# Optimization experiments

Measured on AMD Instinct MI355X. Metric: run time of the kernel, lower is better.

Reference implementation:

```python
import jax, jax.numpy as jnp
import numpy as np

DIM = 512
HEADS = 8
DK = DIM // HEADS
MAX_LEN = 22118
EPS = 1e-5


def _layernorm(h, g, b):
    m = jnp.mean(h, axis=-1, keepdims=True)
    v = jnp.mean((h - m) ** 2, axis=-1, keepdims=True)
    return (h - m) / jnp.sqrt(v + EPS) * g + b


def setup_inputs() -> dict:
    key = jax.random.key(0)
    ks = jax.random.split(key, 16)
    B, S = 4, 2048
    xavier = lambda k, shp: jax.random.normal(k, shp, jnp.float32) * np.sqrt(2.0 / (shp[0] + shp[1]))
    return {
        "x": jax.random.normal(ks[0], (B, S, DIM), jnp.float32),
        "vis_data": jax.random.normal(ks[1], (B, S, DIM), jnp.float32),
        "coord1": jax.random.randint(ks[2], (B, S), 0, MAX_LEN, jnp.int32),
        "coord2": jax.random.randint(ks[3], (B, S), 0, MAX_LEN, jnp.int32),
        "emb1": jax.random.normal(ks[4], (MAX_LEN, DIM // 2), jnp.float32) * 0.02,
        "emb2": jax.random.normal(ks[5], (MAX_LEN, DIM // 2), jnp.float32) * 0.02,
        "wq": xavier(ks[6], (DIM, DIM)), "bq": jnp.zeros((DIM,), jnp.float32),
        "wk": xavier(ks[7], (DIM, DIM)), "bk": jnp.zeros((DIM,), jnp.float32),
        "wv": xavier(ks[8], (DIM, DIM)), "bv": jnp.zeros((DIM,), jnp.float32),
        "w1": xavier(ks[9], (DIM, DIM)), "b1": jnp.zeros((DIM,), jnp.float32),
        "g1": jnp.ones((DIM,), jnp.float32), "beta1": jnp.zeros((DIM,), jnp.float32),
        "w2": xavier(ks[10], (DIM, DIM)), "b2": jnp.zeros((DIM,), jnp.float32),
        "g2": jnp.ones((DIM,), jnp.float32), "beta2": jnp.zeros((DIM,), jnp.float32),
    }


def reference(x, vis_data, coord1, coord2, emb1, emb2, wq, bq, wk, bk, wv, bv,
              w1, b1, g1, beta1, w2, b2, g2, beta2):
    B, S, _ = x.shape
    # learned positional encoding: concat of two coordinate embeddings
    pos = jnp.concatenate([emb1[coord1], emb2[coord2]], axis=-1)  # [B,S,DIM]
    xp = x + pos
    # Q/K from vis_data, V from position-encoded x
    q = (vis_data @ wq + bq).reshape(B, S, HEADS, DK)
    k = (vis_data @ wk + bk).reshape(B, S, HEADS, DK)
    v = (xp @ wv + bv).reshape(B, S, HEADS, DK)
    scores = jnp.einsum("bqhd,bkhd->bhqk", q, k) / np.sqrt(DK).astype(np.float32)
    attn = jax.nn.softmax(scores, axis=-1)  # dropout is identity in eval
    out = jnp.einsum("bhqk,bkhd->bqhd", attn, v).reshape(B, S, DIM)
    # post-attention MLP stack (self.layer)
    h = jax.nn.leaky_relu(out @ w1 + b1, negative_slope=0.2)
    h = _layernorm(h, g1, beta1)
    h = jax.nn.leaky_relu(h @ w2 + b2, negative_slope=0.2)
    h = _layernorm(h, g2, beta2)
    return h
```

## Files before the change

kernel.cpp:

```cpp
#include <hip/hip_runtime.h>

#define DIM 512
#define SEQ 2048
#define MROWS 8192

typedef short short8 __attribute__((ext_vector_type(8)));
typedef float floatx4 __attribute__((ext_vector_type(4)));

__device__ __forceinline__ ushort f2bf(float f) {
  union { float f; unsigned u; } v; v.f = f;
  unsigned r = v.u + 0x7fff + ((v.u >> 16) & 1);
  return (ushort)(r >> 16);
}
__device__ __forceinline__ float bf2f(ushort u) {
  union { unsigned u; float f; } v; v.u = ((unsigned)u) << 16;
  return v.f;
}

__global__ __launch_bounds__(256) void prep_wtrans_kernel(
    const float* __restrict__ x, const float* __restrict__ vis,
    const int* __restrict__ c1, const int* __restrict__ c2,
    const float* __restrict__ e1, const float* __restrict__ e2,
    const float* __restrict__ wq, const float* __restrict__ wk,
    const float* __restrict__ wv, const float* __restrict__ w1,
    const float* __restrict__ w2,
    ushort* __restrict__ xp_bf, ushort* __restrict__ vis_bf,
    ushort* __restrict__ wt_qkv, ushort* __restrict__ wt1,
    ushort* __restrict__ wt2) {
  __shared__ float Ls[64 * 65];
  if (blockIdx.x < 4096) {
    int gid = blockIdx.x * 256 + threadIdx.x;
    int row = gid >> 7;
    int col = (gid & 127) * 4;
    float4 vv = *(const float4*)(vis + (size_t)row * 512 + col);
    ushort4 vb; vb.x = f2bf(vv.x); vb.y = f2bf(vv.y); vb.z = f2bf(vv.z); vb.w = f2bf(vv.w);
    *(ushort4*)(vis_bf + (size_t)row * 512 + col) = vb;
    float4 p;
    if (col < 256) p = *(const float4*)(e1 + (size_t)c1[row] * 256 + col);
    else           p = *(const float4*)(e2 + (size_t)c2[row] * 256 + col - 256);
    float4 xv = *(const float4*)(x + (size_t)row * 512 + col);
    ushort4 xb; xb.x = f2bf(xv.x + p.x); xb.y = f2bf(xv.y + p.y);
    xb.z = f2bf(xv.z + p.z); xb.w = f2bf(xv.w + p.w);
    *(ushort4*)(xp_bf + (size_t)row * 512 + col) = xb;
  } else {
    int bid = blockIdx.x - 4096;
    int mid = bid >> 6;
    int tile = bid & 63;
    int k0 = (tile >> 3) * 64, n0 = (tile & 7) * 64;
    const float* W = mid == 0 ? wq : mid == 1 ? wk : mid == 2 ? wv : mid == 3 ? w1 : w2;
    ushort* outp = mid < 3 ? (wt_qkv + (size_t)mid * 512 * 512) : (mid == 3 ? wt1 : wt2);
    float scale = (mid == 0) ? 0.125f * 1.44269504f : 1.0f;
    int r = threadIdx.x >> 4, c4 = (threadIdx.x & 15) * 4;
#pragma unroll
    for (int i = 0; i < 4; i++) {
      int row = i * 16 + r;
      float4 wv4 = *(const float4*)(W + (size_t)(k0 + row) * 512 + n0 + c4);
      Ls[row * 65 + c4 + 0] = wv4.x * scale;
      Ls[row * 65 + c4 + 1] = wv4.y * scale;
      Ls[row * 65 + c4 + 2] = wv4.z * scale;
      Ls[row * 65 + c4 + 3] = wv4.w * scale;
    }
    __syncthreads();
    int n = threadIdx.x >> 2, kc = (threadIdx.x & 3) * 16;
    ushort pk[16];
#pragma unroll
    for (int i = 0; i < 16; i++) pk[i] = f2bf(Ls[(kc + i) * 65 + n]);
    ushort* op = outp + (size_t)(n0 + n) * 512 + k0 + kc;
    *(uint4*)op = *(uint4*)pk;
    *(uint4*)(op + 8) = *(uint4*)(pk + 8);
  }
}

template <bool LEAKY>
__global__ __launch_bounds__(256, 4) void gemm_mfma(
    const ushort* __restrict__ A01, const ushort* __restrict__ A2,
    const ushort* __restrict__ Wt,
    const float* __restrict__ bias0, const float* __restrict__ bias1,
    const float* __restrict__ bias2,
    ushort* __restrict__ out0, ushort* __restrict__ out1,
    ushort* __restrict__ out2, float s0scale) {
  __shared__ __align__(16) ushort Sm[12288];
  ushort* As = Sm;
  ushort* Bs = Sm + 4096;
  int t = threadIdx.x;
  int seg = blockIdx.x >> 2;
  int nloc0 = (blockIdx.x & 3) * 128;
  int n0w = blockIdx.x * 128;
  int m0 = blockIdx.y * 64;
  const ushort* A = (seg < 2) ? A01 : A2;
  const float* bias = seg == 0 ? bias0 : seg == 1 ? bias1 : bias2;
  ushort* out = seg == 0 ? out0 : seg == 1 ? out1 : out2;
  float bscale = seg == 0 ? s0scale : 1.0f;

  int w = t >> 6, lane = t & 63;
  int wm = (w & 1) * 32, wn = (w >> 1) * 64;
  int quad = lane >> 4, lcol = lane & 15;
  int l8g = lane >> 3, l7g = lane & 7;
  int gchs = (l7g ^ l8g) * 8;

  floatx4 acc[2][4] = {};

  for (int k0 = 0; k0 < 512; k0 += 64) {
    __syncthreads();
#pragma unroll
    for (int i = 0; i < 2; i++) {
      int r0 = w * 16 + i * 8;
      __builtin_amdgcn_global_load_lds(
          (const __attribute__((address_space(1))) unsigned*)(
              A + (size_t)(m0 + r0 + l8g) * 512 + k0 + gchs),
          (__attribute__((address_space(3))) unsigned*)(&As[r0 * 64]),
          16, 0, 0);
    }
#pragma unroll
    for (int i = 0; i < 4; i++) {
      int r0 = w * 32 + i * 8;
      __builtin_amdgcn_global_load_lds(
          (const __attribute__((address_space(1))) unsigned*)(
              Wt + (size_t)(n0w + r0 + l8g) * 512 + k0 + gchs),
          (__attribute__((address_space(3))) unsigned*)(&Bs[r0 * 64]),
          16, 0, 0);
    }
    asm volatile("s_waitcnt vmcnt(0)" ::: "memory");
    __syncthreads();
#pragma unroll
    for (int kc = 0; kc < 2; kc++) {
      int pch = ((kc * 4 + quad) ^ (lcol & 7)) * 8;
      short8 af[2], bfr[4];
#pragma unroll
      for (int i = 0; i < 2; i++)
        af[i] = *(const short8*)(&As[(wm + i * 16 + lcol) * 64 + pch]);
#pragma unroll
      for (int i = 0; i < 4; i++)
        bfr[i] = *(const short8*)(&Bs[(wn + i * 16 + lcol) * 64 + pch]);
#pragma unroll
      for (int mt = 0; mt < 2; mt++)
#pragma unroll
        for (int nt = 0; nt < 4; nt++)
          acc[mt][nt] = __builtin_amdgcn_mfma_f32_16x16x32_bf16(
              af[mt], bfr[nt], acc[mt][nt], 0, 0, 0);
    }
  }

  __syncthreads();
  float* Ls = (float*)Sm + w * 1088;
  int rr = lane >> 2, cc = (lane & 3) * 16;
#pragma unroll
  for (int mt = 0; mt < 2; mt++) {
#pragma unroll
    for (int nt = 0; nt < 4; nt++) {
      float bv = bias[nloc0 + wn + nt * 16 + lcol] * bscale;
#pragma unroll
      for (int r = 0; r < 4; r++) {
        float vv = acc[mt][nt][r] + bv;
        if (LEAKY) vv = vv >= 0.f ? vv : 0.2f * vv;
        Ls[(quad * 4 + r) * 68 + nt * 16 + lcol] = vv;
      }
    }
    asm volatile("s_waitcnt lgkmcnt(0)" ::: "memory");
    ushort pk[16];
#pragma unroll
    for (int i = 0; i < 16; i += 4) {
      float4 fv = *(const float4*)(&Ls[rr * 68 + cc + i]);
      pk[i] = f2bf(fv.x); pk[i + 1] = f2bf(fv.y);
      pk[i + 2] = f2bf(fv.z); pk[i + 3] = f2bf(fv.w);
    }
    ushort* op = out + (size_t)(m0 + wm + mt * 16 + rr) * 512 + nloc0 + wn + cc;
    *(uint4*)op = *(uint4*)pk;
    *(uint4*)(op + 8) = *(uint4*)(pk + 8);
    asm volatile("s_waitcnt lgkmcnt(0)" ::: "memory");
  }
}

__global__ __launch_bounds__(256, 2) void attn_mfma_kernel(
    const ushort* __restrict__ q, const ushort* __restrict__ k,
    const ushort* __restrict__ v, ushort* __restrict__ out) {
  __shared__ __align__(16) ushort Ks[2][128 * 64];
  __shared__ __align__(16) ushort Vt[2][64 * 128];
  __shared__ __align__(16) unsigned Pp[4096];
  int t = threadIdx.x;
  int blk = blockIdx.x;
  blk = ((blk & 7) << 6) | (blk >> 3);
  int qt = blk & 15, h = (blk >> 4) & 7, b = blk >> 7;
  int wave = t >> 6, lane = t & 63, quad = lane >> 4, lcol = lane & 15;
  int q0 = qt * 128 + wave * 32;
  const size_t base = (size_t)b * SEQ * 512 + h * 64;

  short8 qf[2][2];
#pragma unroll
  for (int qm = 0; qm < 2; qm++)
#pragma unroll
    for (int kc = 0; kc < 2; kc++)
      qf[qm][kc] = *(const short8*)(
          q + base + (size_t)(q0 + qm * 16 + lcol) * 512 + kc * 32 + quad * 8);

  floatx4 O[2][4] = {};
  float lsum[2] = {0.f, 0.f};

  unsigned* Ppw = Pp + wave * 1024;
  int pl = t & 63, dg = t >> 6;
  int l8 = lane >> 3, l7 = lane & 7;
  int kchs = (l7 ^ l8) * 8;
  const ushort* vbase = v + base + (size_t)(2 * pl) * 512 + dg * 16;

  uint4 va[2], vb[2];

#pragma unroll
  for (int j = 0; j < 4; j++) {
    const ushort* gp = k + base + (size_t)((wave * 4 + j) * 8 + l8) * 512 + kchs;
    __builtin_amdgcn_global_load_lds(
        (const __attribute__((address_space(1))) unsigned*)gp,
        (__attribute__((address_space(3))) unsigned*)(&Ks[0][(wave * 4 + j) * 512]),
        16, 0, 0);
  }
  va[0] = *(const uint4*)(vbase);       va[1] = *(const uint4*)(vbase + 8);
  vb[0] = *(const uint4*)(vbase + 512); vb[1] = *(const uint4*)(vbase + 520);
  {
    const ushort* a0 = (const ushort*)va;
    const ushort* a1 = (const ushort*)vb;
#pragma unroll
    for (int i = 0; i < 16; i++) {
      int dim = dg * 16 + i;
      unsigned pack = (unsigned)a0[i] | ((unsigned)a1[i] << 16);
      int pch = (pl >> 2) ^ (dim & 7);
      *(unsigned*)(&Vt[0][dim * 128 + pch * 8 + (pl & 3) * 2]) = pack;
    }
  }
  __syncthreads();

  int cb = 0;
  for (int it = 0; it < 16; it++) {
    if (it < 15) {
      int ktn = (it + 1) * 128;
#pragma unroll
      for (int j = 0; j < 4; j++) {
        const ushort* gp =
            k + base + (size_t)(ktn + (wave * 4 + j) * 8 + l8) * 512 + kchs;
        __builtin_amdgcn_global_load_lds(
            (const __attribute__((address_space(1))) unsigned*)gp,
            (__attribute__((address_space(3))) unsigned*)(
                &Ks[cb ^ 1][(wave * 4 + j) * 512]),
            16, 0, 0);
      }
      const ushort* vr = vbase + (size_t)ktn * 512;
      va[0] = *(const uint4*)(vr);       va[1] = *(const uint4*)(vr + 8);
      vb[0] = *(const uint4*)(vr + 512); vb[1] = *(const uint4*)(vr + 520);
    }

    const ushort* Ksb = Ks[cb];
    const ushort* Vtb = Vt[cb];
#pragma unroll
    for (int half = 0; half < 2; half++) {
      short8 kf[2][4];
#pragma unroll
      for (int kc = 0; kc < 2; kc++) {
        int pch = ((kc * 4 + quad) ^ (lcol & 7)) * 8;
#pragma unroll
        for (int jt = 0; jt < 4; jt++)
          kf[kc][jt] =
              *(const short8*)(&Ksb[((half * 4 + jt) * 16 + lcol) * 64 + pch]);
      }
      short8 vf[2][4];
#pragma unroll
      for (int kc = 0; kc < 2; kc++) {
        int ch = half * 8 + kc * 4 + quad;
#pragma unroll
        for (int nt = 0; nt < 4; nt++)
          vf[kc][nt] = *(const short8*)(
              &Vtb[(nt * 16 + lcol) * 128 + ((ch ^ (lcol & 7)) * 8)]);
      }
#pragma unroll
      for (int qm = 0; qm < 2; qm++) {
        floatx4 S[4] = {};
        __builtin_amdgcn_s_setprio(1);
#pragma unroll
        for (int kc = 0; kc < 2; kc++)
#pragma unroll
          for (int jt = 0; jt < 4; jt++)
            S[jt] = __builtin_amdgcn_mfma_f32_16x16x32_bf16(
                kf[kc][jt], qf[qm][kc], S[jt], 0, 0, 0);
        __builtin_amdgcn_s_setprio(0);
#pragma unroll
        for (int jt = 0; jt < 4; jt++) {
          float e0 = exp2f(S[jt][0]);
          float e1 = exp2f(S[jt][1]);
          float e2 = exp2f(S[jt][2]);
          float e3 = exp2f(S[jt][3]);
          lsum[qm] += (e0 + e1) + (e2 + e3);
          unsigned p0, p1;
          asm("v_cvt_pk_bf16_f32 %0, %1, %2" : "=v"(p0) : "v"(e0), "v"(e1));
          asm("v_cvt_pk_bf16_f32 %0, %1, %2" : "=v"(p1) : "v"(e2), "v"(e3));
          int c0 = 2 * jt + (quad >> 1);
          uint2 pk2; pk2.x = p0; pk2.y = p1;
          *(uint2*)(Ppw + qm * 512 + lcol * 32 + ((c0 ^ (lcol & 7)) << 2) +
                    (quad & 1) * 2) = pk2;
        }
      }
      asm volatile("s_waitcnt lgkmcnt(0)" ::: "memory");
      __builtin_amdgcn_sched_barrier(0);
#pragma unroll
      for (int kc = 0; kc < 2; kc++) {
#pragma unroll
        for (int qm = 0; qm < 2; qm++) {
          short8 pf = *(const short8*)(Ppw + qm * 512 + lcol * 32 +
                                       (((kc * 4 + quad) ^ (lcol & 7)) << 2));
          __builtin_amdgcn_s_setprio(1);
#pragma unroll
          for (int nt = 0; nt < 4; nt++)
            O[qm][nt] = __builtin_amdgcn_mfma_f32_16x16x32_bf16(
                vf[kc][nt], pf, O[qm][nt], 0, 0, 0);
          __builtin_amdgcn_s_setprio(0);
        }
      }
    }

    if (it < 15) {
      const ushort* a0 = (const ushort*)va;
      const ushort* a1 = (const ushort*)vb;
      ushort* Vtn = Vt[cb ^ 1];
#pragma unroll
      for (int i = 0; i < 16; i++) {
        int dim = dg * 16 + i;
        unsigned pack = (unsigned)a0[i] | ((unsigned)a1[i] << 16);
        int pch = (pl >> 2) ^ (dim & 7);
        *(unsigned*)(&Vtn[dim * 128 + pch * 8 + (pl & 3) * 2]) = pack;
      }
    }
    asm volatile("s_waitcnt vmcnt(0)" ::: "memory");
    __syncthreads();
    cb ^= 1;
  }

#pragma unroll
  for (int qm = 0; qm < 2; qm++) {
    float s = lsum[qm];
    s += __shfl_xor(s, 16, 64);
    s += __shfl_xor(s, 32, 64);
    float rl = 1.f / s;
#pragma unroll
    for (int nt = 0; nt < 4; nt++) {
      ushort4 o;
      o.x = f2bf(O[qm][nt][0] * rl);
      o.y = f2bf(O[qm][nt][1] * rl);
      o.z = f2bf(O[qm][nt][2] * rl);
      o.w = f2bf(O[qm][nt][3] * rl);
      *(ushort4*)(out + base + (size_t)(q0 + qm * 16 + lcol) * 512 +
                  nt * 16 + quad * 4) = o;
    }
  }
}

template <bool OUTF32>
__global__ __launch_bounds__(256) void ln_kernel(
    const ushort* __restrict__ h, const float* __restrict__ g,
    const float* __restrict__ beta, void* __restrict__ outv) {
  int wave = threadIdx.x >> 6, lane = threadIdx.x & 63;
  int row = blockIdx.x * 4 + wave;
  uint4 raw = *(const uint4*)(h + (size_t)row * 512 + lane * 8);
  const ushort* hu = (const ushort*)&raw;
  float vals[8];
#pragma unroll
  for (int i = 0; i < 8; i++) vals[i] = bf2f(hu[i]);
  float sum = 0.f;
#pragma unroll
  for (int i = 0; i < 8; i++) sum += vals[i];
#pragma unroll
  for (int off = 32; off >= 1; off >>= 1) sum += __shfl_xor(sum, off, 64);
  float mean = sum * (1.f / 512.f);
  float vs = 0.f;
#pragma unroll
  for (int i = 0; i < 8; i++) { float d = vals[i] - mean; vs += d * d; }
#pragma unroll
  for (int off = 32; off >= 1; off >>= 1) vs += __shfl_xor(vs, off, 64);
  float rstd = rsqrtf(vs * (1.f / 512.f) + 1e-5f);
  float4 gv0 = *(const float4*)(g + lane * 8);
  float4 gv1 = *(const float4*)(g + lane * 8 + 4);
  float4 bv0 = *(const float4*)(beta + lane * 8);
  float4 bv1 = *(const float4*)(beta + lane * 8 + 4);
  float gr[8] = {gv0.x, gv0.y, gv0.z, gv0.w, gv1.x, gv1.y, gv1.z, gv1.w};
  float br[8] = {bv0.x, bv0.y, bv0.z, bv0.w, bv1.x, bv1.y, bv1.z, bv1.w};
  float res[8];
#pragma unroll
  for (int i = 0; i < 8; i++) res[i] = (vals[i] - mean) * rstd * gr[i] + br[i];
  if (OUTF32) {
    float* op = (float*)outv + (size_t)row * 512 + lane * 8;
    float4 o0, o1;
    o0.x = res[0]; o0.y = res[1]; o0.z = res[2]; o0.w = res[3];
    o1.x = res[4]; o1.y = res[5]; o1.z = res[6]; o1.w = res[7];
    *(float4*)op = o0; *(float4*)(op + 4) = o1;
  } else {
    ushort* op = (ushort*)outv + (size_t)row * 512 + lane * 8;
    ushort4 o0, o1;
    o0.x = f2bf(res[0]); o0.y = f2bf(res[1]); o0.z = f2bf(res[2]); o0.w = f2bf(res[3]);
    o1.x = f2bf(res[4]); o1.y = f2bf(res[5]); o1.z = f2bf(res[6]); o1.w = f2bf(res[7]);
    *(ushort4*)op = o0; *(ushort4*)(op + 4) = o1;
  }
}

extern "C" void kernel_launch(void* const* d_in, const int* in_sizes, int n_in,
                              void* d_out, int out_size, void* d_ws,
                              size_t ws_size, hipStream_t stream) {
  (void)in_sizes; (void)n_in; (void)out_size; (void)ws_size;
  const float* x     = (const float*)d_in[0];
  const float* vis   = (const float*)d_in[1];
  const int*   c1    = (const int*)d_in[2];
  const int*   c2    = (const int*)d_in[3];
  const float* e1    = (const float*)d_in[4];
  const float* e2    = (const float*)d_in[5];
  const float* wq    = (const float*)d_in[6];
  const float* bq    = (const float*)d_in[7];
  const float* wk    = (const float*)d_in[8];
  const float* bk    = (const float*)d_in[9];
  const float* wv    = (const float*)d_in[10];
  const float* bv    = (const float*)d_in[11];
  const float* w1    = (const float*)d_in[12];
  const float* b1    = (const float*)d_in[13];
  const float* g1    = (const float*)d_in[14];
  const float* beta1 = (const float*)d_in[15];
  const float* w2    = (const float*)d_in[16];
  const float* b2    = (const float*)d_in[17];
  const float* g2    = (const float*)d_in[18];
  const float* beta2 = (const float*)d_in[19];
  float* out = (float*)d_out;
  ushort* ws = (ushort*)d_ws;

  const size_t BUF = (size_t)MROWS * 512;
  ushort* xp_bf  = ws;
  ushort* vis_bf = ws + BUF;
  ushort* q_bf   = ws + 2 * BUF;
  ushort* k_bf   = ws + 3 * BUF;
  ushort* v_bf   = ws + 4 * BUF;
  ushort* wt_qkv = ws + 5 * BUF;
  ushort* wt1    = wt_qkv + 1536 * 512;
  ushort* wt2    = wt1 + 512 * 512;
  ushort* attn_bf = vis_bf;
  ushort* h1_bf   = xp_bf;
  ushort* ln1_bf  = q_bf;
  ushort* h2_bf   = k_bf;

  prep_wtrans_kernel<<<4416, 256, 0, stream>>>(
      x, vis, c1, c2, e1, e2, wq, wk, wv, w1, w2, xp_bf, vis_bf, wt_qkv, wt1, wt2);
  gemm_mfma<false><<<dim3(12, 128), 256, 0, stream>>>(
      vis_bf, xp_bf, wt_qkv, bq, bk, bv, q_bf, k_bf, v_bf, 0.125f * 1.44269504f);
  attn_mfma_kernel<<<512, 256, 0, stream>>>(q_bf, k_bf, v_bf, attn_bf);
  gemm_mfma<true><<<dim3(4, 128), 256, 0, stream>>>(
      attn_bf, attn_bf, wt1, b1, b1, b1, h1_bf, h1_bf, h1_bf, 1.0f);
  ln_kernel<false><<<2048, 256, 0, stream>>>(h1_bf, g1, beta1, ln1_bf);
  gemm_mfma<true><<<dim3(4, 128), 256, 0, stream>>>(
      ln1_bf, ln1_bf, wt2, b2, b2, b2, h2_bf, h2_bf, h2_bf, 1.0f);
  ln_kernel<true><<<2048, 256, 0, stream>>>(h2_bf, g2, beta2, out);
}
```

Measured before the change: 276.5 us.

## Double-buffer GEMM LDS tiles and defer V fragment loads in attention

Result: faster. 266.2 us (-3.7%).

```diff
diff --git a/kernel.cpp b/kernel.cpp
--- a/kernel.cpp
+++ b/kernel.cpp
@@ -79,9 +79,7 @@
     const float* __restrict__ bias2,
     ushort* __restrict__ out0, ushort* __restrict__ out1,
     ushort* __restrict__ out2, float s0scale) {
-  __shared__ __align__(16) ushort Sm[12288];
-  ushort* As = Sm;
-  ushort* Bs = Sm + 4096;
+  __shared__ __align__(16) ushort Sm[24576];
   int t = threadIdx.x;
   int seg = blockIdx.x >> 2;
   int nloc0 = (blockIdx.x & 3) * 128;
@@ -100,28 +98,37 @@
 
   floatx4 acc[2][4] = {};
 
-  for (int k0 = 0; k0 < 512; k0 += 64) {
-    __syncthreads();
-#pragma unroll
-    for (int i = 0; i < 2; i++) {
-      int r0 = w * 16 + i * 8;
-      __builtin_amdgcn_global_load_lds(
-          (const __attribute__((address_space(1))) unsigned*)(
-              A + (size_t)(m0 + r0 + l8g) * 512 + k0 + gchs),
-          (__attribute__((address_space(3))) unsigned*)(&As[r0 * 64]),
-          16, 0, 0);
-    }
-#pragma unroll
-    for (int i = 0; i < 4; i++) {
-      int r0 = w * 32 + i * 8;
-      __builtin_amdgcn_global_load_lds(
-          (const __attribute__((address_space(1))) unsigned*)(
-              Wt + (size_t)(n0w + r0 + l8g) * 512 + k0 + gchs),
-          (__attribute__((address_space(3))) unsigned*)(&Bs[r0 * 64]),
-          16, 0, 0);
-    }
-    asm volatile("s_waitcnt vmcnt(0)" ::: "memory");
-    __syncthreads();
+#define GEMM_STAGE(K0, BUF)                                                   \
+  {                                                                           \
+    ushort* As_ = Sm + (BUF) * 12288;                                         \
+    ushort* Bs_ = As_ + 4096;                                                 \
+    _Pragma("unroll") for (int i = 0; i < 2; i++) {                           \
+      int r0 = w * 16 + i * 8;                                                \
+      __builtin_amdgcn_global_load_lds(                                       \
+          (const __attribute__((address_space(1))) unsigned*)(                \
+              A + (size_t)(m0 + r0 + l8g) * 512 + (K0) + gchs),               \
+          (__attribute__((address_space(3))) unsigned*)(&As_[r0 * 64]),       \
+          16, 0, 0);                                                          \
+    }                                                                         \
+    _Pragma("unroll") for (int i = 0; i < 4; i++) {                           \
+      int r0 = w * 32 + i * 8;                                                \
+      __builtin_amdgcn_global_load_lds(                                       \
+          (const __attribute__((address_space(1))) unsigned*)(                \
+              Wt + (size_t)(n0w + r0 + l8g) * 512 + (K0) + gchs),             \
+          (__attribute__((address_space(3))) unsigned*)(&Bs_[r0 * 64]),       \
+          16, 0, 0);                                                          \
+    }                                                                         \
+  }
+
+  GEMM_STAGE(0, 0);
+  asm volatile("s_waitcnt vmcnt(0)" ::: "memory");
+  __syncthreads();
+
+  for (int ks = 0; ks < 8; ks++) {
+    int cur = ks & 1;
+    if (ks < 7) GEMM_STAGE((ks + 1) * 64, cur ^ 1);
+    const ushort* As = Sm + cur * 12288;
+    const ushort* Bs = As + 4096;
 #pragma unroll
     for (int kc = 0; kc < 2; kc++) {
       int pch = ((kc * 4 + quad) ^ (lcol & 7)) * 8;
@@ -139,9 +146,11 @@
           acc[mt][nt] = __builtin_amdgcn_mfma_f32_16x16x32_bf16(
               af[mt], bfr[nt], acc[mt][nt], 0, 0, 0);
     }
-  }
-
-  __syncthreads();
+    asm volatile("s_waitcnt vmcnt(0)" ::: "memory");
+    __syncthreads();
+  }
+#undef GEMM_STAGE
+
   float* Ls = (float*)Sm + w * 1088;
   int rr = lane >> 2, cc = (lane & 3) * 16;
 #pragma unroll
@@ -258,15 +267,6 @@
         for (int jt = 0; jt < 4; jt++)
           kf[kc][jt] =
               *(const short8*)(&Ksb[((half * 4 + jt) * 16 + lcol) * 64 + pch]);
-      }
-      short8 vf[2][4];
-#pragma unroll
-      for (int kc = 0; kc < 2; kc++) {
-        int ch = half * 8 + kc * 4 + quad;
-#pragma unroll
-        for (int nt = 0; nt < 4; nt++)
-          vf[kc][nt] = *(const short8*)(
-              &Vtb[(nt * 16 + lcol) * 128 + ((ch ^ (lcol & 7)) * 8)]);
       }
 #pragma unroll
       for (int qm = 0; qm < 2; qm++) {
@@ -296,9 +296,14 @@
         }
       }
       asm volatile("s_waitcnt lgkmcnt(0)" ::: "memory");
-      __builtin_amdgcn_sched_barrier(0);
 #pragma unroll
       for (int kc = 0; kc < 2; kc++) {
+        short8 vf[4];
+        int ch = half * 8 + kc * 4 + quad;
+#pragma unroll
+        for (int nt = 0; nt < 4; nt++)
+          vf[nt] = *(const short8*)(
+              &Vtb[(nt * 16 + lcol) * 128 + ((ch ^ (lcol & 7)) * 8)]);
 #pragma unroll
         for (int qm = 0; qm < 2; qm++) {
           short8 pf = *(const short8*)(Ppw + qm * 512 + lcol * 32 +
@@ -307,7 +312,7 @@
 #pragma unroll
           for (int nt = 0; nt < 4; nt++)
             O[qm][nt] = __builtin_amdgcn_mfma_f32_16x16x32_bf16(
-                vf[kc][nt], pf, O[qm][nt], 0, 0, 0);
+                vf[nt], pf, O[qm][nt], 0, 0, 0);
           __builtin_amdgcn_s_setprio(0);
         }
       }
```
